# Performance work log

Measured on AMD Instinct MI355X. Metric: run time of the kernel, lower is better.

The kernel has to match this reference:

```python
import jax, jax.numpy as jnp
import numpy as np

HIDDEN = 512
NUM_HEADS = 8


def setup_inputs() -> dict:
    key = jax.random.key(0)
    ks = jax.random.split(key, 8)
    Tq, Tk, Cq, Ck, H = 1, 65536, 512, 512, HIDDEN
    s = 1.0 / np.sqrt(H)
    return {
        "Q": jax.random.normal(ks[0], (Tq, Cq), jnp.float32),
        "K": jax.random.normal(ks[1], (Tk, Ck), jnp.float32),
        "Wq": jax.random.normal(ks[2], (H, Cq), jnp.float32) * s,
        "bq": jax.random.normal(ks[3], (H,), jnp.float32) * s,
        "Wk": jax.random.normal(ks[4], (H, Ck), jnp.float32) * s,
        "bk": jax.random.normal(ks[5], (H,), jnp.float32) * s,
        "Wout": jax.random.normal(ks[6], (1, NUM_HEADS), jnp.float32) * 0.3,
        "bout": jax.random.normal(ks[7], (1,), jnp.float32) * 0.3,
    }


def reference(Q, K, Wq, bq, Wk, bk, Wout, bout):
    h = NUM_HEADS
    H = Wq.shape[0]
    d = H // h  # per-head dim
    # linear + ReLU projections
    Ql = jax.nn.relu(Q @ Wq.T + bq)          # [1, H]
    Kl = jax.nn.relu(K @ Wk.T + bk)          # [Tk, H]
    # split into heads (T_q == 1 is required by linear_out)
    Qh = Ql.reshape(h, d)                    # [h, d]
    Kh = Kl.reshape(-1, h, d)                # [Tk, h, d]
    # per-head scores, scaled by sqrt(d_head); dropout rate 0 -> identity
    scores = jnp.einsum('hd,thd->th', Qh, Kh) / (d ** 0.5)  # [Tk, h]
    # learned per-head fusion, then softmax over the T_k axis
    logits = scores @ Wout.T + bout          # [Tk, 1]
    return jax.nn.softmax(logits, axis=0)    # [Tk, 1]
```

## Files before the change

### kernel.cpp

```cpp
#include <hip/hip_runtime.h>
#include <hip/hip_fp16.h>

#define CDIM  512
#define ROWS  65536
#define TILES 16
#define GX    128
#define NCLS  4

typedef _Float16 half8  __attribute__((ext_vector_type(8)));
typedef __fp16   fp16x2 __attribute__((ext_vector_type(2)));
typedef float    f32x16 __attribute__((ext_vector_type(16)));

__global__ void qproj_kernel(const float* __restrict__ Q, const float* __restrict__ Wq,
                             const float* __restrict__ bq, const float* __restrict__ Wout,
                             float* __restrict__ v) {
    __shared__ float qs[CDIM];
    const int t = threadIdx.x;
    qs[t] = Q[t]; qs[t + 256] = Q[t + 256];
    __syncthreads();
    const int jj  = t >> 4;
    const int sub = t & 15;
    const int j   = blockIdx.x * 16 + jj;
    const float4* w4 = (const float4*)(Wq + (size_t)j * CDIM + sub * 32);
    const float4* q4 = (const float4*)(qs + sub * 32);
    float s = 0.f;
    #pragma unroll
    for (int i = 0; i < 8; ++i) {
        float4 w = w4[i]; float4 q = q4[i];
        s = fmaf(w.x, q.x, s); s = fmaf(w.y, q.y, s);
        s = fmaf(w.z, q.z, s); s = fmaf(w.w, q.w, s);
    }
    s += __shfl_xor(s, 1); s += __shfl_xor(s, 2);
    s += __shfl_xor(s, 4); s += __shfl_xor(s, 8);
    if (sub == 0) {
        s += bq[j];
        s = fmaxf(s, 0.f);
        v[j] = s * Wout[j >> 6] * 0.125f;
    }
}

__global__ void wkfrag_kernel(const float* __restrict__ Wk, _Float16* __restrict__ Wkf) {
    const int gid = blockIdx.x * 256 + threadIdx.x;
    const int jb  = gid >> 11;
    const int kc  = (gid >> 6) & 31;
    const int l   = gid & 63;
    const int j   = jb * 32 + (l & 31);
    const int k   = kc * 16 + (l >> 5) * 8;
    const float* src = Wk + (size_t)j * CDIM + k;
    float4 f0 = *(const float4*)(src);
    float4 f1 = *(const float4*)(src + 4);
    half8 h;
    h[0]=(_Float16)f0.x; h[1]=(_Float16)f0.y; h[2]=(_Float16)f0.z; h[3]=(_Float16)f0.w;
    h[4]=(_Float16)f1.x; h[5]=(_Float16)f1.y; h[6]=(_Float16)f1.z; h[7]=(_Float16)f1.w;
    *(half8*)(Wkf + (size_t)gid * 8) = h;
}

__global__ __launch_bounds__(256, 2) void score_kernel(
    const float* __restrict__ Kmat, const _Float16* __restrict__ Wkf,
    const float* __restrict__ bk, const float* __restrict__ v,
    float* __restrict__ partial2)
{
    __shared__ alignas(16) _Float16 stage[2][32][512];
    __shared__ float scratch2[2][4][32];

    const int tid  = threadIdx.x;
    const int lane = tid & 63;
    const int wave = tid >> 6;
    const int l31  = lane & 31;
    const int lhi  = lane >> 5;
    const int cls  = blockIdx.y;
    const int jb   = cls * 4 + wave;

    half8 B[32];
    const half8* bsrc = (const half8*)Wkf + (size_t)jb * 2048 + lane;
    #pragma unroll
    for (int kc = 0; kc < 32; ++kc) B[kc] = bsrc[kc * 64];
    const int jmy = jb * 32 + l31;
    const float bj = bk[jmy];
    const float vj = v[jmy];

    const int rowbase = blockIdx.x * (TILES * 32);
    float* pbase = partial2 + (size_t)cls * ROWS;

    {
        #pragma unroll
        for (int i = 0; i < 8; ++i) {
            const int rt = wave * 8 + i;
            const float* src = Kmat + (size_t)(rowbase + rt) * CDIM + lane * 8;
            float4 a = *(const float4*)(src);
            float4 b = *(const float4*)(src + 4);
            union { fp16x2 h2[4]; half8 h8; } u;
            u.h2[0] = __builtin_amdgcn_cvt_pkrtz(a.x, a.y);
            u.h2[1] = __builtin_amdgcn_cvt_pkrtz(a.z, a.w);
            u.h2[2] = __builtin_amdgcn_cvt_pkrtz(b.x, b.y);
            u.h2[3] = __builtin_amdgcn_cvt_pkrtz(b.z, b.w);
            const int slot = lane ^ (rt & 7);
            *(half8*)(&stage[0][rt][slot * 8]) = u.h8;
        }
    }
    __syncthreads();

    for (int t = 0; t < TILES; ++t) {
        const int cur = t & 1;
        const bool pf = (t + 1 < TILES);

        if (t > 0 && tid < 32) {
            const int pt = (t - 1) & 1;
            float s = scratch2[pt][0][tid] + scratch2[pt][1][tid]
                    + scratch2[pt][2][tid] + scratch2[pt][3][tid];
            pbase[rowbase + (t - 1) * 32 + tid] = s;
        }

        f32x16 acc0, acc1;
        #pragma unroll
        for (int r = 0; r < 16; ++r) { acc0[r] = 0.f; acc1[r] = 0.f; }

        const _Float16* sb = &stage[cur][0][0];

        float4 ga0[4], gb0[4];
        if (pf) {
            const int rs = rowbase + (t + 1) * 32;
            #pragma unroll
            for (int i = 0; i < 4; ++i) {
                const float* src = Kmat + (size_t)(rs + wave * 8 + i) * CDIM + lane * 8;
                ga0[i] = *(const float4*)(src);
                gb0[i] = *(const float4*)(src + 4);
            }
        }
        __builtin_amdgcn_sched_barrier(0);

        #pragma unroll
        for (int kc = 0; kc < 16; kc += 2) {
            const int ch0 = (kc * 2 + lhi) ^ (l31 & 7);
            const int ch1 = ((kc + 1) * 2 + lhi) ^ (l31 & 7);
            half8 a0 = *(const half8*)(sb + l31 * 512 + ch0 * 8);
            half8 a1 = *(const half8*)(sb + l31 * 512 + ch1 * 8);
            acc0 = __builtin_amdgcn_mfma_f32_32x32x16_f16(a0, B[kc],     acc0, 0, 0, 0);
            acc1 = __builtin_amdgcn_mfma_f32_32x32x16_f16(a1, B[kc + 1], acc1, 0, 0, 0);
        }

        if (pf) {
            #pragma unroll
            for (int i = 0; i < 4; ++i) {
                const int rt = wave * 8 + i;
                union { fp16x2 h2[4]; half8 h8; } u;
                u.h2[0] = __builtin_amdgcn_cvt_pkrtz(ga0[i].x, ga0[i].y);
                u.h2[1] = __builtin_amdgcn_cvt_pkrtz(ga0[i].z, ga0[i].w);
                u.h2[2] = __builtin_amdgcn_cvt_pkrtz(gb0[i].x, gb0[i].y);
                u.h2[3] = __builtin_amdgcn_cvt_pkrtz(gb0[i].z, gb0[i].w);
                const int slot = lane ^ (rt & 7);
                *(half8*)(&stage[cur ^ 1][rt][slot * 8]) = u.h8;
            }
        }

        float4 ga1[4], gb1[4];
        if (pf) {
            const int rs = rowbase + (t + 1) * 32;
            #pragma unroll
            for (int i = 0; i < 4; ++i) {
                const float* src = Kmat + (size_t)(rs + wave * 8 + 4 + i) * CDIM + lane * 8;
                ga1[i] = *(const float4*)(src);
                gb1[i] = *(const float4*)(src + 4);
            }
        }
        __builtin_amdgcn_sched_barrier(0);

        #pragma unroll
        for (int kc = 16; kc < 32; kc += 2) {
            const int ch0 = (kc * 2 + lhi) ^ (l31 & 7);
            const int ch1 = ((kc + 1) * 2 + lhi) ^ (l31 & 7);
            half8 a0 = *(const half8*)(sb + l31 * 512 + ch0 * 8);
            half8 a1 = *(const half8*)(sb + l31 * 512 + ch1 * 8);
            acc0 = __builtin_amdgcn_mfma_f32_32x32x16_f16(a0, B[kc],     acc0, 0, 0, 0);
            acc1 = __builtin_amdgcn_mfma_f32_32x32x16_f16(a1, B[kc + 1], acc1, 0, 0, 0);
        }

        if (pf) {
            #pragma unroll
            for (int i = 0; i < 4; ++i) {
                const int rt = wave * 8 + 4 + i;
                union { fp16x2 h2[4]; half8 h8; } u;
                u.h2[0] = __builtin_amdgcn_cvt_pkrtz(ga1[i].x, ga1[i].y);
                u.h2[1] = __builtin_amdgcn_cvt_pkrtz(ga1[i].z, ga1[i].w);
                u.h2[2] = __builtin_amdgcn_cvt_pkrtz(gb1[i].x, gb1[i].y);
                u.h2[3] = __builtin_amdgcn_cvt_pkrtz(gb1[i].z, gb1[i].w);
                const int slot = lane ^ (rt & 7);
                *(half8*)(&stage[cur ^ 1][rt][slot * 8]) = u.h8;
            }
        }

        float x[16];
        #pragma unroll
        for (int r = 0; r < 16; ++r)
            x[r] = fmaxf(acc0[r] + acc1[r] + bj, 0.f) * vj;

        float q0[8];
        #pragma unroll
        for (int i = 0; i < 8; ++i) {
            const bool b = lane & 1;
            float keep = b ? x[i + 8] : x[i];
            float send = b ? x[i] : x[i + 8];
            q0[i] = keep + __shfl_xor(send, 1);
        }
        float q1[4];
        #pragma unroll
        for (int i = 0; i < 4; ++i) {
            const bool b = lane & 2;
            float keep = b ? q0[i + 4] : q0[i];
            float send = b ? q0[i] : q0[i + 4];
            q1[i] = keep + __shfl_xor(send, 2);
        }
        float q2[2];
        #pragma unroll
        for (int i = 0; i < 2; ++i) {
            const bool b = lane & 4;
            float keep = b ? q1[i + 2] : q1[i];
            float send = b ? q1[i] : q1[i + 2];
            q2[i] = keep + __shfl_xor(send, 4);
        }
        float q3;
        {
            const bool b = lane & 8;
            float keep = b ? q2[1] : q2[0];
            float send = b ? q2[0] : q2[1];
            q3 = keep + __shfl_xor(send, 8);
        }
        float s = q3 + __shfl_xor(q3, 16);
        if (l31 < 16) {
            const int r   = ((l31 & 1) << 3) | ((l31 & 2) << 1) | ((l31 & 4) >> 1) | ((l31 & 8) >> 3);
            const int row = (r & 3) + 8 * (r >> 2) + 4 * lhi;
            scratch2[cur][wave][row] = s;
        }

        __syncthreads();
    }

    if (tid < 32) {
        const int pt = (TILES - 1) & 1;
        float s = scratch2[pt][0][tid] + scratch2[pt][1][tid]
                + scratch2[pt][2][tid] + scratch2[pt][3][tid];
        pbase[rowbase + (TILES - 1) * 32 + tid] = s;
    }
}

__global__ void expsum_kernel(const float* __restrict__ partial2, float* __restrict__ logits,
                              float* __restrict__ blocksum) {
    __shared__ float red[256];
    const int t = threadIdx.x;
    const int row = blockIdx.x * 256 + t;
    const float lg = partial2[row] + partial2[ROWS + row]
                   + partial2[2 * ROWS + row] + partial2[3 * ROWS + row];
    logits[row] = lg;
    red[t] = expf(lg);
    __syncthreads();
    for (int s = 128; s > 0; s >>= 1) {
        if (t < s) red[t] += red[t + s];
        __syncthreads();
    }
    if (t == 0) blocksum[blockIdx.x] = red[0];
}

__global__ void norm_kernel(const float* __restrict__ logits, const float* __restrict__ blocksum,
                            float* __restrict__ out) {
    __shared__ float red[256];
    const int t = threadIdx.x;
    red[t] = blocksum[t];
    __syncthreads();
    for (int s = 128; s > 0; s >>= 1) {
        if (t < s) red[t] += red[t + s];
        __syncthreads();
    }
    const float zinv = 1.0f / red[0];
    const int i = blockIdx.x * 256 + t;
    out[i] = expf(logits[i]) * zinv;
}

extern "C" void kernel_launch(void* const* d_in, const int* in_sizes, int n_in,
                              void* d_out, int out_size, void* d_ws, size_t ws_size,
                              hipStream_t stream) {
    const float* Q    = (const float*)d_in[0];
    const float* Kmat = (const float*)d_in[1];
    const float* Wq   = (const float*)d_in[2];
    const float* bq   = (const float*)d_in[3];
    const float* Wk   = (const float*)d_in[4];
    const float* bk   = (const float*)d_in[5];
    const float* Wout = (const float*)d_in[6];
    float* out = (float*)d_out;

    char* ws = (char*)d_ws;
    _Float16* Wkf   = (_Float16*)(ws);
    float* v        = (float*)(ws + 524288);
    float* partial2 = (float*)(ws + 526336);
    float* logits   = (float*)(ws + 1574912);
    float* blocksum = (float*)(ws + 1837056);

    hipLaunchKernelGGL(qproj_kernel,  dim3(32),        dim3(256), 0, stream, Q, Wq, bq, Wout, v);
    hipLaunchKernelGGL(wkfrag_kernel, dim3(128),       dim3(256), 0, stream, Wk, Wkf);
    hipLaunchKernelGGL(score_kernel,  dim3(GX, NCLS),  dim3(256), 0, stream, Kmat, Wkf, bk, v, partial2);
    hipLaunchKernelGGL(expsum_kernel, dim3(256),       dim3(256), 0, stream, partial2, logits, blocksum);
    hipLaunchKernelGGL(norm_kernel,   dim3(256),       dim3(256), 0, stream, logits, blocksum, out);
}
```

Measured before the change: 64.43 us.

## Widen score blocks to 8 waves and 64-row tiles to halve K rereads

The score kernel now uses 512-thread blocks covering 256 hidden units each, so only two column classes re-read the large K matrix instead of four. Tiles grow to 64 rows, letting each wave reuse its register-held Wk fragments across two MFMA row blocks. Staging uses a byte-swizzled layout with 8 threads per row, and block ids are remapped so paired classes run close together. The trade-off is larger LDS use per block (likely one block per CU) and fewer waves in flight to hide global latency.

```diff
diff --git a/kernel.cpp b/kernel.cpp
--- a/kernel.cpp
+++ b/kernel.cpp
@@ -3,9 +3,8 @@
 
 #define CDIM  512
 #define ROWS  65536
-#define TILES 16
-#define GX    128
-#define NCLS  4
+#define TILES 8
+#define TR    64
 
 typedef _Float16 half8  __attribute__((ext_vector_type(8)));
 typedef __fp16   fp16x2 __attribute__((ext_vector_type(2)));
@@ -55,21 +54,24 @@
     *(half8*)(Wkf + (size_t)gid * 8) = h;
 }
 
-__global__ __launch_bounds__(256, 2) void score_kernel(
+__global__ __launch_bounds__(512, 2) void score_kernel(
     const float* __restrict__ Kmat, const _Float16* __restrict__ Wkf,
     const float* __restrict__ bk, const float* __restrict__ v,
     float* __restrict__ partial2)
 {
-    __shared__ alignas(16) _Float16 stage[2][32][512];
-    __shared__ float scratch2[2][4][32];
+    __shared__ alignas(16) char stage[2][TR * 1024];
+    __shared__ float scratch2[2][8][TR];
 
     const int tid  = threadIdx.x;
     const int lane = tid & 63;
     const int wave = tid >> 6;
     const int l31  = lane & 31;
     const int lhi  = lane >> 5;
-    const int cls  = blockIdx.y;
-    const int jb   = cls * 4 + wave;
+
+    const int bid      = blockIdx.x;
+    const int rowblock = (bid & 7) * 16 + (bid >> 4);
+    const int cls      = (bid >> 3) & 1;
+    const int jb       = cls * 8 + wave;
 
     half8 B[32];
     const half8* bsrc = (const half8*)Wkf + (size_t)jb * 2048 + lane;
@@ -79,23 +81,29 @@
     const float bj = bk[jmy];
     const float vj = v[jmy];
 
-    const int rowbase = blockIdx.x * (TILES * 32);
+    const int rowbase = rowblock * (TILES * TR);
     float* pbase = partial2 + (size_t)cls * ROWS;
 
-    {
-        #pragma unroll
-        for (int i = 0; i < 8; ++i) {
-            const int rt = wave * 8 + i;
-            const float* src = Kmat + (size_t)(rowbase + rt) * CDIM + lane * 8;
-            float4 a = *(const float4*)(src);
-            float4 b = *(const float4*)(src + 4);
+    const int srow = tid >> 3;
+    const int sc8  = tid & 7;
+    const int swz  = (srow & 7) << 4;
+    const char* gbase = (const char*)(Kmat + (size_t)(rowbase + srow) * CDIM + sc8 * 64);
+    char* lbase0;
+
+    #pragma unroll
+    for (int h = 0; h < 2; ++h) {
+        float4 L[8];
+        #pragma unroll
+        for (int i = 0; i < 8; ++i)
+            L[i] = *(const float4*)(gbase + (size_t)h * 128 + i * 16);
+        #pragma unroll
+        for (int s = 0; s < 4; ++s) {
             union { fp16x2 h2[4]; half8 h8; } u;
-            u.h2[0] = __builtin_amdgcn_cvt_pkrtz(a.x, a.y);
-            u.h2[1] = __builtin_amdgcn_cvt_pkrtz(a.z, a.w);
-            u.h2[2] = __builtin_amdgcn_cvt_pkrtz(b.x, b.y);
-            u.h2[3] = __builtin_amdgcn_cvt_pkrtz(b.z, b.w);
-            const int slot = lane ^ (rt & 7);
-            *(half8*)(&stage[0][rt][slot * 8]) = u.h8;
+            u.h2[0] = __builtin_amdgcn_cvt_pkrtz(L[2*s].x,   L[2*s].y);
+            u.h2[1] = __builtin_amdgcn_cvt_pkrtz(L[2*s].z,   L[2*s].w);
+            u.h2[2] = __builtin_amdgcn_cvt_pkrtz(L[2*s+1].x, L[2*s+1].y);
+            u.h2[3] = __builtin_amdgcn_cvt_pkrtz(L[2*s+1].z, L[2*s+1].w);
+            *(half8*)(&stage[0][srow * 1024 + ((sc8 * 128 + h * 64 + s * 16) ^ swz)]) = u.h8;
         }
     }
     __syncthreads();
@@ -103,143 +111,131 @@
     for (int t = 0; t < TILES; ++t) {
         const int cur = t & 1;
         const bool pf = (t + 1 < TILES);
-
-        if (t > 0 && tid < 32) {
+        const char* sb = &stage[cur][0];
+        char* db = &stage[cur ^ 1][0];
+        const char* gt = gbase + (size_t)(t + 1) * TR * CDIM * 4;
+
+        if (t > 0 && tid < TR) {
             const int pt = (t - 1) & 1;
-            float s = scratch2[pt][0][tid] + scratch2[pt][1][tid]
-                    + scratch2[pt][2][tid] + scratch2[pt][3][tid];
-            pbase[rowbase + (t - 1) * 32 + tid] = s;
+            float s = 0.f;
+            #pragma unroll
+            for (int w = 0; w < 8; ++w) s += scratch2[pt][w][tid];
+            pbase[rowbase + (t - 1) * TR + tid] = s;
         }
 
         f32x16 acc0, acc1;
         #pragma unroll
         for (int r = 0; r < 16; ++r) { acc0[r] = 0.f; acc1[r] = 0.f; }
 
-        const _Float16* sb = &stage[cur][0][0];
-
-        float4 ga0[4], gb0[4];
+        float4 L[8];
         if (pf) {
-            const int rs = rowbase + (t + 1) * 32;
+            #pragma unroll
+            for (int i = 0; i < 8; ++i) L[i] = *(const float4*)(gt + i * 16);
+        }
+        __builtin_amdgcn_sched_barrier(0);
+
+        const int rswz = (l31 & 7) << 4;
+        #pragma unroll
+        for (int kc = 0; kc < 16; ++kc) {
+            const int off = (kc * 32 + lhi * 16) ^ rswz;
+            half8 a0 = *(const half8*)(sb + l31 * 1024 + off);
+            half8 a1 = *(const half8*)(sb + (32 + l31) * 1024 + off);
+            acc0 = __builtin_amdgcn_mfma_f32_32x32x16_f16(a0, B[kc], acc0, 0, 0, 0);
+            acc1 = __builtin_amdgcn_mfma_f32_32x32x16_f16(a1, B[kc], acc1, 0, 0, 0);
+        }
+
+        if (pf) {
+            #pragma unroll
+            for (int s = 0; s < 4; ++s) {
+                union { fp16x2 h2[4]; half8 h8; } u;
+                u.h2[0] = __builtin_amdgcn_cvt_pkrtz(L[2*s].x,   L[2*s].y);
+                u.h2[1] = __builtin_amdgcn_cvt_pkrtz(L[2*s].z,   L[2*s].w);
+                u.h2[2] = __builtin_amdgcn_cvt_pkrtz(L[2*s+1].x, L[2*s+1].y);
+                u.h2[3] = __builtin_amdgcn_cvt_pkrtz(L[2*s+1].z, L[2*s+1].w);
+                *(half8*)(db + srow * 1024 + ((sc8 * 128 + s * 16) ^ swz)) = u.h8;
+            }
+            #pragma unroll
+            for (int i = 0; i < 8; ++i) L[i] = *(const float4*)(gt + 128 + i * 16);
+        }
+        __builtin_amdgcn_sched_barrier(0);
+
+        #pragma unroll
+        for (int kc = 16; kc < 32; ++kc) {
+            const int off = (kc * 32 + lhi * 16) ^ rswz;
+            half8 a0 = *(const half8*)(sb + l31 * 1024 + off);
+            half8 a1 = *(const half8*)(sb + (32 + l31) * 1024 + off);
+            acc0 = __builtin_amdgcn_mfma_f32_32x32x16_f16(a0, B[kc], acc0, 0, 0, 0);
+            acc1 = __builtin_amdgcn_mfma_f32_32x32x16_f16(a1, B[kc], acc1, 0, 0, 0);
+        }
+
+        if (pf) {
+            #pragma unroll
+            for (int s = 0; s < 4; ++s) {
+                union { fp16x2 h2[4]; half8 h8; } u;
+                u.h2[0] = __builtin_amdgcn_cvt_pkrtz(L[2*s].x,   L[2*s].y);
+                u.h2[1] = __builtin_amdgcn_cvt_pkrtz(L[2*s].z,   L[2*s].w);
+                u.h2[2] = __builtin_amdgcn_cvt_pkrtz(L[2*s+1].x, L[2*s+1].y);
+                u.h2[3] = __builtin_amdgcn_cvt_pkrtz(L[2*s+1].z, L[2*s+1].w);
+                *(half8*)(db + srow * 1024 + ((sc8 * 128 + 64 + s * 16) ^ swz)) = u.h8;
+            }
+        }
+
+        #pragma unroll
+        for (int g = 0; g < 2; ++g) {
+            float x[16];
+            #pragma unroll
+            for (int r = 0; r < 16; ++r) {
+                float a = (g == 0) ? acc0[r] : acc1[r];
+                x[r] = fmaxf(a + bj, 0.f) * vj;
+            }
+            float q0[8];
+            #pragma unroll
+            for (int i = 0; i < 8; ++i) {
+                const bool b = lane & 1;
+                float keep = b ? x[i + 8] : x[i];
+                float send = b ? x[i] : x[i + 8];
+                q0[i] = keep + __shfl_xor(send, 1);
+            }
+            float q1[4];
             #pragma unroll
             for (int i = 0; i < 4; ++i) {
-                const float* src = Kmat + (size_t)(rs + wave * 8 + i) * CDIM + lane * 8;
-                ga0[i] = *(const float4*)(src);
-                gb0[i] = *(const float4*)(src + 4);
-            }
-        }
-        __builtin_amdgcn_sched_barrier(0);
-
-        #pragma unroll
-        for (int kc = 0; kc < 16; kc += 2) {
-            const int ch0 = (kc * 2 + lhi) ^ (l31 & 7);
-            const int ch1 = ((kc + 1) * 2 + lhi) ^ (l31 & 7);
-            half8 a0 = *(const half8*)(sb + l31 * 512 + ch0 * 8);
-            half8 a1 = *(const half8*)(sb + l31 * 512 + ch1 * 8);
-            acc0 = __builtin_amdgcn_mfma_f32_32x32x16_f16(a0, B[kc],     acc0, 0, 0, 0);
-            acc1 = __builtin_amdgcn_mfma_f32_32x32x16_f16(a1, B[kc + 1], acc1, 0, 0, 0);
-        }
-
-        if (pf) {
-            #pragma unroll
-            for (int i = 0; i < 4; ++i) {
-                const int rt = wave * 8 + i;
-                union { fp16x2 h2[4]; half8 h8; } u;
-                u.h2[0] = __builtin_amdgcn_cvt_pkrtz(ga0[i].x, ga0[i].y);
-                u.h2[1] = __builtin_amdgcn_cvt_pkrtz(ga0[i].z, ga0[i].w);
-                u.h2[2] = __builtin_amdgcn_cvt_pkrtz(gb0[i].x, gb0[i].y);
-                u.h2[3] = __builtin_amdgcn_cvt_pkrtz(gb0[i].z, gb0[i].w);
-                const int slot = lane ^ (rt & 7);
-                *(half8*)(&stage[cur ^ 1][rt][slot * 8]) = u.h8;
-            }
-        }
-
-        float4 ga1[4], gb1[4];
-        if (pf) {
-            const int rs = rowbase + (t + 1) * 32;
-            #pragma unroll
-            for (int i = 0; i < 4; ++i) {
-                const float* src = Kmat + (size_t)(rs + wave * 8 + 4 + i) * CDIM + lane * 8;
-                ga1[i] = *(const float4*)(src);
-                gb1[i] = *(const float4*)(src + 4);
-            }
-        }
-        __builtin_amdgcn_sched_barrier(0);
-
-        #pragma unroll
-        for (int kc = 16; kc < 32; kc += 2) {
-            const int ch0 = (kc * 2 + lhi) ^ (l31 & 7);
-            const int ch1 = ((kc + 1) * 2 + lhi) ^ (l31 & 7);
-            half8 a0 = *(const half8*)(sb + l31 * 512 + ch0 * 8);
-            half8 a1 = *(const half8*)(sb + l31 * 512 + ch1 * 8);
-            acc0 = __builtin_amdgcn_mfma_f32_32x32x16_f16(a0, B[kc],     acc0, 0, 0, 0);
-            acc1 = __builtin_amdgcn_mfma_f32_32x32x16_f16(a1, B[kc + 1], acc1, 0, 0, 0);
-        }
-
-        if (pf) {
-            #pragma unroll
-            for (int i = 0; i < 4; ++i) {
-                const int rt = wave * 8 + 4 + i;
-                union { fp16x2 h2[4]; half8 h8; } u;
-                u.h2[0] = __builtin_amdgcn_cvt_pkrtz(ga1[i].x, ga1[i].y);
-                u.h2[1] = __builtin_amdgcn_cvt_pkrtz(ga1[i].z, ga1[i].w);
-                u.h2[2] = __builtin_amdgcn_cvt_pkrtz(gb1[i].x, gb1[i].y);
-                u.h2[3] = __builtin_amdgcn_cvt_pkrtz(gb1[i].z, gb1[i].w);
-                const int slot = lane ^ (rt & 7);
-                *(half8*)(&stage[cur ^ 1][rt][slot * 8]) = u.h8;
-            }
-        }
-
-        float x[16];
-        #pragma unroll
-        for (int r = 0; r < 16; ++r)
-            x[r] = fmaxf(acc0[r] + acc1[r] + bj, 0.f) * vj;
-
-        float q0[8];
-        #pragma unroll
-        for (int i = 0; i < 8; ++i) {
-            const bool b = lane & 1;
-            float keep = b ? x[i + 8] : x[i];
-            float send = b ? x[i] : x[i + 8];
-            q0[i] = keep + __shfl_xor(send, 1);
-        }
-        float q1[4];
-        #pragma unroll
-        for (int i = 0; i < 4; ++i) {
-            const bool b = lane & 2;
-            float keep = b ? q0[i + 4] : q0[i];
-            float send = b ? q0[i] : q0[i + 4];
-            q1[i] = keep + __shfl_xor(send, 2);
-        }
-        float q2[2];
-        #pragma unroll
-        for (int i = 0; i < 2; ++i) {
-            const bool b = lane & 4;
-            float keep = b ? q1[i + 2] : q1[i];
-            float send = b ? q1[i] : q1[i + 2];
-            q2[i] = keep + __shfl_xor(send, 4);
-        }
-        float q3;
-        {
-            const bool b = lane & 8;
-            float keep = b ? q2[1] : q2[0];
-            float send = b ? q2[0] : q2[1];
-            q3 = keep + __shfl_xor(send, 8);
-        }
-        float s = q3 + __shfl_xor(q3, 16);
-        if (l31 < 16) {
-            const int r   = ((l31 & 1) << 3) | ((l31 & 2) << 1) | ((l31 & 4) >> 1) | ((l31 & 8) >> 3);
-            const int row = (r & 3) + 8 * (r >> 2) + 4 * lhi;
-            scratch2[cur][wave][row] = s;
+                const bool b = lane & 2;
+                float keep = b ? q0[i + 4] : q0[i];
+                float send = b ? q0[i] : q0[i + 4];
+                q1[i] = keep + __shfl_xor(send, 2);
+            }
+            float q2[2];
+            #pragma unroll
+            for (int i = 0; i < 2; ++i) {
+                const bool b = lane & 4;
+                float keep = b ? q1[i + 2] : q1[i];
+                float send = b ? q1[i] : q1[i + 2];
+                q2[i] = keep + __shfl_xor(send, 4);
+            }
+            float q3;
+            {
+                const bool b = lane & 8;
+                float keep = b ? q2[1] : q2[0];
+                float send = b ? q2[0] : q2[1];
+                q3 = keep + __shfl_xor(send, 8);
+            }
+            float s = q3 + __shfl_xor(q3, 16);
+            if (l31 < 16) {
+                const int r   = ((l31 & 1) << 3) | ((l31 & 2) << 1) | ((l31 & 4) >> 1) | ((l31 & 8) >> 3);
+                const int row = (r & 3) + 8 * (r >> 2) + 4 * lhi;
+                scratch2[cur][wave][g * 32 + row] = s;
+            }
         }
 
         __syncthreads();
     }
 
-    if (tid < 32) {
+    if (tid < TR) {
         const int pt = (TILES - 1) & 1;
-        float s = scratch2[pt][0][tid] + scratch2[pt][1][tid]
-                + scratch2[pt][2][tid] + scratch2[pt][3][tid];
-        pbase[rowbase + (TILES - 1) * 32 + tid] = s;
+        float s = 0.f;
+        #pragma unroll
+        for (int w = 0; w < 8; ++w) s += scratch2[pt][w][tid];
+        pbase[rowbase + (TILES - 1) * TR + tid] = s;
     }
 }
 
@@ -248,8 +244,7 @@
     __shared__ float red[256];
     const int t = threadIdx.x;
     const int row = blockIdx.x * 256 + t;
-    const float lg = partial2[row] + partial2[ROWS + row]
-                   + partial2[2 * ROWS + row] + partial2[3 * ROWS + row];
+    const float lg = partial2[row] + partial2[ROWS + row];
     logits[row] = lg;
     red[t] = expf(lg);
     __syncthreads();
@@ -291,12 +286,12 @@
     _Float16* Wkf   = (_Float16*)(ws);
     float* v        = (float*)(ws + 524288);
     float* partial2 = (float*)(ws + 526336);
-    float* logits   = (float*)(ws + 1574912);
-    float* blocksum = (float*)(ws + 1837056);
-
-    hipLaunchKernelGGL(qproj_kernel,  dim3(32),        dim3(256), 0, stream, Q, Wq, bq, Wout, v);
-    hipLaunchKernelGGL(wkfrag_kernel, dim3(128),       dim3(256), 0, stream, Wk, Wkf);
-    hipLaunchKernelGGL(score_kernel,  dim3(GX, NCLS),  dim3(256), 0, stream, Kmat, Wkf, bk, v, partial2);
-    hipLaunchKernelGGL(expsum_kernel, dim3(256),       dim3(256), 0, stream, partial2, logits, blocksum);
-    hipLaunchKernelGGL(norm_kernel,   dim3(256),       dim3(256), 0, stream, logits, blocksum, out);
-}
+    float* logits   = (float*)(ws + 1050624);
+    float* blocksum = (float*)(ws + 1312768);
+
+    hipLaunchKernelGGL(qproj_kernel,  dim3(32),   dim3(256), 0, stream, Q, Wq, bq, Wout, v);
+    hipLaunchKernelGGL(wkfrag_kernel, dim3(128),  dim3(256), 0, stream, Wk, Wkf);
+    hipLaunchKernelGGL(score_kernel,  dim3(256),  dim3(512), 0, stream, Kmat, Wkf, bk, v, partial2);
+    hipLaunchKernelGGL(expsum_kernel, dim3(256),  dim3(256), 0, stream, partial2, logits, blocksum);
+    hipLaunchKernelGGL(norm_kernel,   dim3(256),  dim3(256), 0, stream, logits, blocksum, out);
+}
```

New measurement: 77.59 us. +20.4%, slower.
